# Kernel optimization log

Measured on AMD Instinct MI355X. Metric: run time of the kernel, lower is better.

The kernel has to match this reference:

```python
import jax, jax.numpy as jnp
import numpy as np

N_NODES = 100000
N_EDGES = 640000
D_IN = 128
D_OUT = 128


def setup_inputs() -> dict:
    key = jax.random.key(0)
    k1, k2, k3, k4 = jax.random.split(key, 4)
    x = jax.random.normal(k1, (N_NODES, D_IN), dtype=jnp.float32)
    edge_index = jax.random.randint(k2, (2, N_EDGES), 0, N_NODES, dtype=jnp.int64)
    # nn.Linear(input_dim, out_dim): weight [out, in], bias [out]
    bound = 1.0 / np.sqrt(D_IN)
    W = jax.random.uniform(k3, (D_OUT, D_IN), minval=-bound, maxval=bound, dtype=jnp.float32)
    b = jax.random.uniform(k4, (D_OUT,), minval=-bound, maxval=bound, dtype=jnp.float32)
    return {"x": x, "edge_index": edge_index, "W": W, "b": b}


def reference(x, edge_index, W, b):
    # GINConv (eps=0): h_i = (1+eps)*x_i + sum_{j in N(i)} x_j, then Linear(h)
    src = edge_index[0]
    dst = edge_index[1]
    agg = jax.ops.segment_sum(x[src], dst, num_segments=N_NODES)  # [N, D_IN]
    h = x + agg
    return h @ W.T + b  # [N, D_OUT]
```

## Files before the change

### kernel.cpp

```cpp
#include <hip/hip_runtime.h>
#include <hip/hip_bf16.h>

#define N_NODES 100000
#define N_EDGES 640000
#define D 128
#define NBINS 782
#define NBINSP 784
#define CHB 320
#define CHE 2000
#define CAP 2048
#define GB 1563
#define TB (GB + CHB)

typedef __attribute__((ext_vector_type(8))) short short8;
typedef __attribute__((ext_vector_type(4))) float f32x4;

__device__ __forceinline__ short f32_to_bf16(float f) {
  union { float f; unsigned u; } c; c.f = f;
  unsigned u = c.u;
  unsigned r = (u + 0x7FFFu + ((u >> 16) & 1u)) >> 16;
  return (short)r;
}
__device__ __forceinline__ float lo_bf16(unsigned v) {
  union { unsigned u; float f; } c; c.u = v << 16; return c.f;
}
__device__ __forceinline__ float hi_bf16(unsigned v) {
  union { unsigned u; float f; } c; c.u = v & 0xFFFF0000u; return c.f;
}

__global__ __launch_bounds__(256) void gemm_count(const float* x, const float* W,
                                                  const int* ei, short* y, int* hist) {
  __shared__ char ldsbuf[128 * 136 * 2];
  int b = blockIdx.x;
  int g_incl = ((b + 1) * GB) / TB;
  bool is_gemm = g_incl > (b * GB) / TB;
  int t = threadIdx.x;

  if (!is_gemm) {
    int* h = (int*)ldsbuf;
    int sid = b - g_incl;
    for (int j = t; j < NBINSP; j += 256) h[j] = 0;
    __syncthreads();
    int base = sid * CHE;
    for (int i = t; i < CHE; i += 256) {
      int dst = ei[N_EDGES + base + i];
      atomicAdd(&h[dst >> 7], 1);
    }
    __syncthreads();
    for (int j = t; j < NBINSP; j += 256) hist[sid * NBINSP + j] = h[j];
    return;
  }

  short (*Wlds)[136] = (short(*)[136])ldsbuf;
  int gb = g_incl - 1;
  for (int idx = t * 8; idx < D * D; idx += 256 * 8) {
    int r = idx >> 7, c = idx & 127;
    float4 a = *reinterpret_cast<const float4*>(W + idx);
    float4 bb = *reinterpret_cast<const float4*>(W + idx + 4);
    short8 s;
    s[0] = f32_to_bf16(a.x);  s[1] = f32_to_bf16(a.y);
    s[2] = f32_to_bf16(a.z);  s[3] = f32_to_bf16(a.w);
    s[4] = f32_to_bf16(bb.x); s[5] = f32_to_bf16(bb.y);
    s[6] = f32_to_bf16(bb.z); s[7] = f32_to_bf16(bb.w);
    *reinterpret_cast<short8*>(&Wlds[r][c]) = s;
  }
  __syncthreads();

  int wave = t >> 6, lane = t & 63;
  int l15 = lane & 15, kq = lane >> 4;
  int row0 = gb * 64 + wave * 16;
  if (row0 >= N_NODES) return;
  int ar = row0 + l15;
  if (ar >= N_NODES) ar = N_NODES - 1;
  const float* xrow = x + (size_t)ar * D;

  f32x4 acc[8];
#pragma unroll
  for (int n = 0; n < 8; ++n) acc[n] = (f32x4){0.f, 0.f, 0.f, 0.f};

#pragma unroll
  for (int kk = 0; kk < 4; ++kk) {
    int k0 = kk * 32 + kq * 8;
    float4 a0 = *reinterpret_cast<const float4*>(xrow + k0);
    float4 a1 = *reinterpret_cast<const float4*>(xrow + k0 + 4);
    short8 af;
    af[0] = f32_to_bf16(a0.x); af[1] = f32_to_bf16(a0.y);
    af[2] = f32_to_bf16(a0.z); af[3] = f32_to_bf16(a0.w);
    af[4] = f32_to_bf16(a1.x); af[5] = f32_to_bf16(a1.y);
    af[6] = f32_to_bf16(a1.z); af[7] = f32_to_bf16(a1.w);
#pragma unroll
    for (int n = 0; n < 8; ++n) {
      short8 bf = *reinterpret_cast<short8*>(&Wlds[n * 16 + l15][k0]);
      acc[n] = __builtin_amdgcn_mfma_f32_16x16x32_bf16(af, bf, acc[n], 0, 0, 0);
    }
  }

  int orow0 = row0 + kq * 4;
#pragma unroll
  for (int n = 0; n < 8; ++n) {
#pragma unroll
    for (int r = 0; r < 4; ++r) {
      int row = orow0 + r;
      if (row < N_NODES)
        y[(size_t)row * D + n * 16 + l15] = f32_to_bf16(acc[n][r]);
    }
  }
}

__global__ __launch_bounds__(256) void scan_cols(const int* hist, int* scanned, int* bintot) {
  __shared__ int sdata[256];
  int j = blockIdx.x;
  int t = threadIdx.x;
  int a = 0, b = 0;
  if (t < CHB / 2) {
    a = hist[(2 * t) * NBINSP + j];
    b = hist[(2 * t + 1) * NBINSP + j];
  }
  int ps = a + b;
  sdata[t] = ps;
  __syncthreads();
  int incl = ps;
  for (int off = 1; off < 256; off <<= 1) {
    int u = (t >= off) ? sdata[t - off] : 0;
    __syncthreads();
    incl += u;
    sdata[t] = incl;
    __syncthreads();
  }
  if (t < CHB / 2) {
    int excl = incl - ps;
    scanned[j * CHB + 2 * t] = excl;
    scanned[j * CHB + 2 * t + 1] = excl + a;
  }
  if (t == CHB / 2 - 1) bintot[j] = incl;
}

__global__ __launch_bounds__(256) void scan_bins(const int* bintot, int* bases) {
  __shared__ int sdata[256];
  int t = threadIdx.x;
  int v0 = 0, v1 = 0, v2 = 0, v3 = 0;
  if (t < NBINSP / 4) {
    int4 vv = *reinterpret_cast<const int4*>(bintot + 4 * t);
    v0 = vv.x; v1 = vv.y; v2 = vv.z; v3 = vv.w;
  }
  int s = v0 + v1 + v2 + v3;
  sdata[t] = s;
  __syncthreads();
  int incl = s;
  for (int off = 1; off < 256; off <<= 1) {
    int u = (t >= off) ? sdata[t - off] : 0;
    __syncthreads();
    incl += u;
    sdata[t] = incl;
    __syncthreads();
  }
  if (t < NBINSP / 4) {
    int e = incl - s;
    bases[4 * t + 0] = e;
    bases[4 * t + 1] = e + v0;
    bases[4 * t + 2] = e + v0 + v1;
    bases[4 * t + 3] = e + v0 + v1 + v2;
  }
  if (t == NBINSP / 4 - 1) bases[NBINSP] = incl;
}

__global__ __launch_bounds__(256) void bin_place(const int* ei, const int* scanned,
                                                 const int* bases, int* binned) {
  __shared__ int rk[NBINSP];
  __shared__ int cb[NBINSP];
  int t = threadIdx.x, b = blockIdx.x;
  for (int j = t; j < NBINSP; j += 256) {
    rk[j] = 0;
    cb[j] = bases[j] + scanned[j * CHB + b];
  }
  __syncthreads();
  int base = b * CHE;
  for (int i = t; i < CHE; i += 256) {
    int e = base + i;
    int src = ei[e];
    int dst = ei[N_EDGES + e];
    int bin = dst >> 7;
    int r = atomicAdd(&rk[bin], 1);
    binned[cb[bin] + r] = ((dst & 127) << 17) | src;
  }
}

__global__ __launch_bounds__(256) void sort_bins(const int* binned, const int* bases,
                                                 int* csr, int* nstart, int* ndeg) {
  __shared__ int c[128];
  __shared__ int st[128];
  __shared__ int sdata[128];
  int bin = blockIdx.x, t = threadIdx.x;
  int est = bases[bin];
  int E = bases[bin + 1] - est;
  if (E > CAP) E = CAP;
  if (t < 128) c[t] = 0;
  __syncthreads();

  int pv[8], rv[8];
#pragma unroll
  for (int j = 0; j < 8; ++j) {
    int i = j * 256 + t;
    bool v = i < E;
    int p = v ? binned[est + i] : 0;
    pv[j] = p;
    rv[j] = v ? atomicAdd(&c[p >> 17], 1) : 0;
  }
  __syncthreads();

  if (t < 128) sdata[t] = c[t];
  __syncthreads();
  int incl = (t < 128) ? sdata[t] : 0;
  for (int off = 1; off < 128; off <<= 1) {
    int u = (t >= off && t < 128) ? sdata[t - off] : 0;
    __syncthreads();
    if (t < 128) {
      incl += u;
      sdata[t] = incl;
    }
    __syncthreads();
  }
  if (t < 128) {
    st[t] = incl - c[t];
    int gnode = bin * 128 + t;
    if (gnode < N_NODES) {
      nstart[gnode] = est + st[t];
      ndeg[gnode] = c[t];
    }
  }
  __syncthreads();

#pragma unroll
  for (int j = 0; j < 8; ++j) {
    int i = j * 256 + t;
    if (i < E) {
      int p = pv[j];
      csr[est + st[p >> 17] + rv[j]] = p & 0x1FFFF;
    }
  }
}

__global__ __launch_bounds__(256) void gather_csr(const short* y, const int* nstart,
                                                  const int* ndeg, const int* csr,
                                                  const float* bias, float* out) {
  int gtid = blockIdx.x * 256 + threadIdx.x;
  int wave = gtid >> 6;
  int lane = threadIdx.x & 63;
  int g = lane >> 5;
  int l = lane & 31;
  int node = wave * 2 + g;

  int deg = ndeg[node];
  int start = nstart[node];
  int dcap = deg < 32 ? deg : 32;
  int docap = __shfl_xor(dcap, 32);
  int kmaxw = dcap > docap ? dcap : docap;

  int ids = (l < dcap) ? csr[start + l] : 0;
  int base_sl = lane & 32;

  const uint2* yq = (const uint2*)y;
  uint2 self = yq[(size_t)node * 32 + l];

  float4 acc[8];
#pragma unroll
  for (int i = 0; i < 8; ++i) acc[i] = make_float4(0.f, 0.f, 0.f, 0.f);

  for (int k = 0; k < kmaxw; k += 8) {
#pragma unroll
    for (int i = 0; i < 8; ++i) {
      int kk = k + i;
      int src = __shfl(ids, base_sl + kk);
      uint2 w = yq[(size_t)src * 32 + l];
      bool val = kk < dcap;
      w.x = val ? w.x : 0u;
      w.y = val ? w.y : 0u;
      acc[i].x += lo_bf16(w.x);
      acc[i].y += hi_bf16(w.x);
      acc[i].z += lo_bf16(w.y);
      acc[i].w += hi_bf16(w.y);
    }
  }
  for (int k = 32; k < deg; ++k) {
    int src = csr[start + k];
    uint2 w = yq[(size_t)src * 32 + l];
    acc[0].x += lo_bf16(w.x);
    acc[0].y += hi_bf16(w.x);
    acc[0].z += lo_bf16(w.y);
    acc[0].w += hi_bf16(w.y);
  }

  float4 bv = ((const float4*)bias)[l];
  float4 tot;
  tot.x = (lo_bf16(self.x) + bv.x) + (((acc[0].x + acc[1].x) + (acc[2].x + acc[3].x)) +
                                      ((acc[4].x + acc[5].x) + (acc[6].x + acc[7].x)));
  tot.y = (hi_bf16(self.x) + bv.y) + (((acc[0].y + acc[1].y) + (acc[2].y + acc[3].y)) +
                                      ((acc[4].y + acc[5].y) + (acc[6].y + acc[7].y)));
  tot.z = (lo_bf16(self.y) + bv.z) + (((acc[0].z + acc[1].z) + (acc[2].z + acc[3].z)) +
                                      ((acc[4].z + acc[5].z) + (acc[6].z + acc[7].z)));
  tot.w = (hi_bf16(self.y) + bv.w) + (((acc[0].w + acc[1].w) + (acc[2].w + acc[3].w)) +
                                      ((acc[4].w + acc[5].w) + (acc[6].w + acc[7].w)));

  ((float4*)out)[(size_t)node * 32 + l] = tot;
}

__global__ void copy_x(const float4* x, float4* h, int n4) {
  int i = blockIdx.x * blockDim.x + threadIdx.x;
  int s = gridDim.x * blockDim.x;
  for (; i < n4; i += s) h[i] = x[i];
}

__global__ void scatter_add(const float* x, const int* ei, float* h) {
  int i = blockIdx.x * blockDim.x + threadIdx.x;
  int s = gridDim.x * blockDim.x;
  const int total = N_EDGES * 32;
  for (; i < total; i += s) {
    int e = i >> 5;
    int c = (i & 31) << 2;
    int src = ei[e];
    int dst = ei[N_EDGES + e];
    float4 v = *reinterpret_cast<const float4*>(x + (size_t)src * D + c);
    float* hp = h + (size_t)dst * D + c;
    unsafeAtomicAdd(hp + 0, v.x);
    unsafeAtomicAdd(hp + 1, v.y);
    unsafeAtomicAdd(hp + 2, v.z);
    unsafeAtomicAdd(hp + 3, v.w);
  }
}

__global__ __launch_bounds__(256) void gin_gemm_f32(const float* h, const float* W,
                                                    const float* bias, float* out) {
  __shared__ short Wlds[128][136];
  int t = threadIdx.x;
  for (int idx = t * 8; idx < D * D; idx += 256 * 8) {
    int r = idx >> 7, c = idx & 127;
    float4 a = *reinterpret_cast<const float4*>(W + idx);
    float4 b = *reinterpret_cast<const float4*>(W + idx + 4);
    short8 s;
    s[0] = f32_to_bf16(a.x); s[1] = f32_to_bf16(a.y);
    s[2] = f32_to_bf16(a.z); s[3] = f32_to_bf16(a.w);
    s[4] = f32_to_bf16(b.x); s[5] = f32_to_bf16(b.y);
    s[6] = f32_to_bf16(b.z); s[7] = f32_to_bf16(b.w);
    *reinterpret_cast<short8*>(&Wlds[r][c]) = s;
  }
  __syncthreads();

  int wave = t >> 6, lane = t & 63;
  int l15 = lane & 15, kq = lane >> 4;
  int row0 = blockIdx.x * 64 + wave * 16;
  if (row0 >= N_NODES) return;
  int ar = row0 + l15;
  if (ar >= N_NODES) ar = N_NODES - 1;
  const float* hrow = h + (size_t)ar * D;

  f32x4 acc[8];
#pragma unroll
  for (int n = 0; n < 8; ++n) acc[n] = (f32x4){0.f, 0.f, 0.f, 0.f};

#pragma unroll
  for (int kk = 0; kk < 4; ++kk) {
    int k0 = kk * 32 + kq * 8;
    float4 a0 = *reinterpret_cast<const float4*>(hrow + k0);
    float4 a1 = *reinterpret_cast<const float4*>(hrow + k0 + 4);
    short8 af;
    af[0] = f32_to_bf16(a0.x); af[1] = f32_to_bf16(a0.y);
    af[2] = f32_to_bf16(a0.z); af[3] = f32_to_bf16(a0.w);
    af[4] = f32_to_bf16(a1.x); af[5] = f32_to_bf16(a1.y);
    af[6] = f32_to_bf16(a1.z); af[7] = f32_to_bf16(a1.w);
#pragma unroll
    for (int n = 0; n < 8; ++n) {
      short8 bf = *reinterpret_cast<short8*>(&Wlds[n * 16 + l15][k0]);
      acc[n] = __builtin_amdgcn_mfma_f32_16x16x32_bf16(af, bf, acc[n], 0, 0, 0);
    }
  }

  int orow0 = row0 + kq * 4;
#pragma unroll
  for (int n = 0; n < 8; ++n) {
    float bv = bias[n * 16 + l15];
#pragma unroll
    for (int r = 0; r < 4; ++r) {
      int row = orow0 + r;
      if (row < N_NODES)
        out[(size_t)row * D + n * 16 + l15] = acc[n][r] + bv;
    }
  }
}

extern "C" void kernel_launch(void* const* d_in, const int* in_sizes, int n_in,
                              void* d_out, int out_size, void* d_ws, size_t ws_size,
                              hipStream_t stream) {
  const float* x   = (const float*)d_in[0];
  const int*   ei  = (const int*)d_in[1];
  const float* W   = (const float*)d_in[2];
  const float* bia = (const float*)d_in[3];
  float* out = (float*)d_out;
  (void)in_sizes; (void)n_in; (void)out_size;

  const size_t HIST_I   = (size_t)CHB * NBINSP;
  const size_t SCAN_I   = (size_t)NBINSP * CHB;
  const size_t BINTOT_I = NBINSP;
  const size_t BASES_I  = 800;
  const size_t BINNED_I = N_EDGES;
  const size_t CSR_I    = N_EDGES;
  const size_t NST_I    = N_NODES;
  const size_t NDG_I    = N_NODES;
  const size_t INTS = HIST_I + SCAN_I + BINTOT_I + BASES_I + BINNED_I + CSR_I + NST_I + NDG_I;
  const size_t Y_B  = (size_t)N_NODES * D * 2;
  const size_t NEED = INTS * 4 + Y_B;

  if (ws_size >= NEED) {
    int* hist    = (int*)d_ws;
    int* scanned = hist + HIST_I;
    int* bintot  = scanned + SCAN_I;
    int* bases   = bintot + BINTOT_I;
    int* binned  = bases + BASES_I;
    int* csr     = binned + BINNED_I;
    int* nstart  = csr + CSR_I;
    int* ndeg    = nstart + NST_I;
    short* y     = (short*)(ndeg + NDG_I);

    gemm_count<<<TB, 256, 0, stream>>>(x, W, ei, y, hist);
    scan_cols<<<NBINSP, 256, 0, stream>>>(hist, scanned, bintot);
    scan_bins<<<1, 256, 0, stream>>>(bintot, bases);
    bin_place<<<CHB, 256, 0, stream>>>(ei, scanned, bases, binned);
    sort_bins<<<NBINS, 256, 0, stream>>>(binned, bases, csr, nstart, ndeg);
    gather_csr<<<(N_NODES / 2) / 4, 256, 0, stream>>>(y, nstart, ndeg, csr, bia, out);
  } else {
    int n4 = N_NODES * D / 4;
    copy_x<<<(n4 + 255) / 256, 256, 0, stream>>>((const float4*)x, (float4*)out, n4);
    int total = N_EDGES * 32;
    scatter_add<<<(total + 255) / 256, 256, 0, stream>>>(x, ei, out);
    gin_gemm_f32<<<(N_NODES + 63) / 64, 256, 0, stream>>>(out, W, bia, out);
  }
}
```

Measured before the change: 89.66 us.

## Distribute GEMM tiles across all CSR-build phase kernels to fill idle CUs

```diff
diff --git a/kernel.cpp b/kernel.cpp
--- a/kernel.cpp
+++ b/kernel.cpp
@@ -9,8 +9,12 @@
 #define CHB 320
 #define CHE 2000
 #define CAP 2048
-#define GB 1563
-#define TB (GB + CHB)
+#define GBT 1563
+#define G1 300
+#define G2 300
+#define G3 200
+#define G4 350
+#define G5 413
 
 typedef __attribute__((ext_vector_type(8))) short short8;
 typedef __attribute__((ext_vector_type(4))) float f32x4;
@@ -28,31 +32,10 @@
   union { unsigned u; float f; } c; c.u = v & 0xFFFF0000u; return c.f;
 }
 
-__global__ __launch_bounds__(256) void gemm_count(const float* x, const float* W,
-                                                  const int* ei, short* y, int* hist) {
-  __shared__ char ldsbuf[128 * 136 * 2];
-  int b = blockIdx.x;
-  int g_incl = ((b + 1) * GB) / TB;
-  bool is_gemm = g_incl > (b * GB) / TB;
-  int t = threadIdx.x;
-
-  if (!is_gemm) {
-    int* h = (int*)ldsbuf;
-    int sid = b - g_incl;
-    for (int j = t; j < NBINSP; j += 256) h[j] = 0;
-    __syncthreads();
-    int base = sid * CHE;
-    for (int i = t; i < CHE; i += 256) {
-      int dst = ei[N_EDGES + base + i];
-      atomicAdd(&h[dst >> 7], 1);
-    }
-    __syncthreads();
-    for (int j = t; j < NBINSP; j += 256) hist[sid * NBINSP + j] = h[j];
-    return;
-  }
-
+__device__ __forceinline__ void gemm_body(const float* x, const float* W, short* y,
+                                          int gb, char* ldsbuf) {
   short (*Wlds)[136] = (short(*)[136])ldsbuf;
-  int gb = g_incl - 1;
+  int t = threadIdx.x;
   for (int idx = t * 8; idx < D * D; idx += 256 * 8) {
     int r = idx >> 7, c = idx & 127;
     float4 a = *reinterpret_cast<const float4*>(W + idx);
@@ -107,16 +90,47 @@
   }
 }
 
-__global__ __launch_bounds__(256) void scan_cols(const int* hist, int* scanned, int* bintot) {
-  __shared__ int sdata[256];
-  int j = blockIdx.x;
-  int t = threadIdx.x;
-  int a = 0, b = 0;
+#define HETERO_MAP(S_, G_)                                   \
+  int b = blockIdx.x;                                        \
+  int g_incl = ((b + 1) * (G_)) / ((S_) + (G_));             \
+  bool is_gemm = g_incl > (b * (G_)) / ((S_) + (G_));        \
+  int sid = b - g_incl;                                      \
+  int gb_loc = g_incl - 1;
+
+__global__ __launch_bounds__(256) void p1_count(const float* x, const float* W, short* y,
+                                                const int* ei, int* hist) {
+  __shared__ char ldsbuf[34816];
+  HETERO_MAP(CHB, G1)
+  int t = threadIdx.x;
+  if (is_gemm) { gemm_body(x, W, y, gb_loc, ldsbuf); return; }
+
+  int* h = (int*)ldsbuf;
+  for (int j = t; j < NBINSP; j += 256) h[j] = 0;
+  __syncthreads();
+  int base = sid * CHE;
+  for (int i = t; i < CHE; i += 256) {
+    int dst = ei[N_EDGES + base + i];
+    atomicAdd(&h[dst >> 7], 1);
+  }
+  __syncthreads();
+  for (int j = t; j < NBINSP; j += 256) hist[sid * NBINSP + j] = h[j];
+}
+
+__global__ __launch_bounds__(256) void p2_scancols(const float* x, const float* W, short* y,
+                                                   const int* hist, int* scanned, int* bintot) {
+  __shared__ char ldsbuf[34816];
+  HETERO_MAP(NBINSP, G2)
+  int t = threadIdx.x;
+  if (is_gemm) { gemm_body(x, W, y, G1 + gb_loc, ldsbuf); return; }
+
+  int* sdata = (int*)ldsbuf;
+  int j = sid;
+  int a = 0, bb = 0;
   if (t < CHB / 2) {
     a = hist[(2 * t) * NBINSP + j];
-    b = hist[(2 * t + 1) * NBINSP + j];
-  }
-  int ps = a + b;
+    bb = hist[(2 * t + 1) * NBINSP + j];
+  }
+  int ps = a + bb;
   sdata[t] = ps;
   __syncthreads();
   int incl = ps;
@@ -135,9 +149,14 @@
   if (t == CHB / 2 - 1) bintot[j] = incl;
 }
 
-__global__ __launch_bounds__(256) void scan_bins(const int* bintot, int* bases) {
-  __shared__ int sdata[256];
-  int t = threadIdx.x;
+__global__ __launch_bounds__(256) void p3_scanbins(const float* x, const float* W, short* y,
+                                                   const int* bintot, int* bases) {
+  __shared__ char ldsbuf[34816];
+  int b = blockIdx.x;
+  int t = threadIdx.x;
+  if (b > 0) { gemm_body(x, W, y, G1 + G2 + b - 1, ldsbuf); return; }
+
+  int* sdata = (int*)ldsbuf;
   int v0 = 0, v1 = 0, v2 = 0, v3 = 0;
   if (t < NBINSP / 4) {
     int4 vv = *reinterpret_cast<const int4*>(bintot + 4 * t);
@@ -164,17 +183,22 @@
   if (t == NBINSP / 4 - 1) bases[NBINSP] = incl;
 }
 
-__global__ __launch_bounds__(256) void bin_place(const int* ei, const int* scanned,
-                                                 const int* bases, int* binned) {
-  __shared__ int rk[NBINSP];
-  __shared__ int cb[NBINSP];
-  int t = threadIdx.x, b = blockIdx.x;
+__global__ __launch_bounds__(256) void p4_place(const float* x, const float* W, short* y,
+                                                const int* ei, const int* scanned,
+                                                const int* bases, int* binned) {
+  __shared__ char ldsbuf[34816];
+  HETERO_MAP(CHB, G4)
+  int t = threadIdx.x;
+  if (is_gemm) { gemm_body(x, W, y, G1 + G2 + G3 + gb_loc, ldsbuf); return; }
+
+  int* rk = (int*)ldsbuf;
+  int* cb = rk + NBINSP;
   for (int j = t; j < NBINSP; j += 256) {
     rk[j] = 0;
-    cb[j] = bases[j] + scanned[j * CHB + b];
-  }
-  __syncthreads();
-  int base = b * CHE;
+    cb[j] = bases[j] + scanned[j * CHB + sid];
+  }
+  __syncthreads();
+  int base = sid * CHE;
   for (int i = t; i < CHE; i += 256) {
     int e = base + i;
     int src = ei[e];
@@ -185,12 +209,18 @@
   }
 }
 
-__global__ __launch_bounds__(256) void sort_bins(const int* binned, const int* bases,
-                                                 int* csr, int* nstart, int* ndeg) {
-  __shared__ int c[128];
-  __shared__ int st[128];
-  __shared__ int sdata[128];
-  int bin = blockIdx.x, t = threadIdx.x;
+__global__ __launch_bounds__(256) void p5_sort(const float* x, const float* W, short* y,
+                                               const int* binned, const int* bases,
+                                               int* csr, int* nstart, int* ndeg) {
+  __shared__ char ldsbuf[34816];
+  HETERO_MAP(NBINS, G5)
+  int t = threadIdx.x;
+  if (is_gemm) { gemm_body(x, W, y, G1 + G2 + G3 + G4 + gb_loc, ldsbuf); return; }
+
+  int* c = (int*)ldsbuf;
+  int* st = c + 128;
+  int* sdata = st + 128;
+  int bin = sid;
   int est = bases[bin];
   int E = bases[bin + 1] - est;
   if (E > CAP) E = CAP;
@@ -420,12 +450,12 @@
     int* ndeg    = nstart + NST_I;
     short* y     = (short*)(ndeg + NDG_I);
 
-    gemm_count<<<TB, 256, 0, stream>>>(x, W, ei, y, hist);
-    scan_cols<<<NBINSP, 256, 0, stream>>>(hist, scanned, bintot);
-    scan_bins<<<1, 256, 0, stream>>>(bintot, bases);
-    bin_place<<<CHB, 256, 0, stream>>>(ei, scanned, bases, binned);
-    sort_bins<<<NBINS, 256, 0, stream>>>(binned, bases, csr, nstart, ndeg);
-    gather_csr<<<(N_NODES / 2) / 4, 256, 0, stream>>>(y, nstart, ndeg, csr, bia, out);
+    p1_count   <<<CHB + G1,    256, 0, stream>>>(x, W, y, ei, hist);
+    p2_scancols<<<NBINSP + G2, 256, 0, stream>>>(x, W, y, hist, scanned, bintot);
+    p3_scanbins<<<1 + G3,      256, 0, stream>>>(x, W, y, bintot, bases);
+    p4_place   <<<CHB + G4,    256, 0, stream>>>(x, W, y, ei, scanned, bases, binned);
+    p5_sort    <<<NBINS + G5,  256, 0, stream>>>(x, W, y, binned, bases, csr, nstart, ndeg);
+    gather_csr <<<(N_NODES / 2) / 4, 256, 0, stream>>>(y, nstart, ndeg, csr, bia, out);
   } else {
     int n4 = N_NODES * D / 4;
     copy_x<<<(n4 + 255) / 256, 256, 0, stream>>>((const float4*)x, (float4*)out, n4);
```

Measured after the change: 96.24 us. +7.3%, slower.

## Replace CSR with fixed 32-slot padded adjacency and zero-row sentinel

Applied to the files above, without the earlier changes.

```diff
diff --git a/kernel.cpp b/kernel.cpp
--- a/kernel.cpp
+++ b/kernel.cpp
@@ -11,6 +11,8 @@
 #define CAP 2048
 #define GB 1563
 #define TB (GB + CHB)
+#define ZROW N_NODES
+#define CSRN (NBINS * 128)
 
 typedef __attribute__((ext_vector_type(8))) short short8;
 typedef __attribute__((ext_vector_type(4))) float f32x4;
@@ -135,9 +137,11 @@
   if (t == CHB / 2 - 1) bintot[j] = incl;
 }
 
-__global__ __launch_bounds__(256) void scan_bins(const int* bintot, int* bases) {
+__global__ __launch_bounds__(256) void scan_bins(const int* bintot, int* bases, short* y) {
   __shared__ int sdata[256];
   int t = threadIdx.x;
+  if (t < 64) ((int*)(y + (size_t)ZROW * D))[t] = 0;
+
   int v0 = 0, v1 = 0, v2 = 0, v3 = 0;
   if (t < NBINSP / 4) {
     int4 vv = *reinterpret_cast<const int4*>(bintot + 4 * t);
@@ -185,64 +189,43 @@
   }
 }
 
-__global__ __launch_bounds__(256) void sort_bins(const int* binned, const int* bases,
-                                                 int* csr, int* nstart, int* ndeg) {
+__global__ __launch_bounds__(256) void sort_bins32(const int* binned, const int* bases,
+                                                   int* csr32, int* ndeg) {
   __shared__ int c[128];
-  __shared__ int st[128];
-  __shared__ int sdata[128];
   int bin = blockIdx.x, t = threadIdx.x;
+  if (t < 128) c[t] = 0;
+  __syncthreads();
   int est = bases[bin];
   int E = bases[bin + 1] - est;
   if (E > CAP) E = CAP;
-  if (t < 128) c[t] = 0;
-  __syncthreads();
-
-  int pv[8], rv[8];
-#pragma unroll
-  for (int j = 0; j < 8; ++j) {
-    int i = j * 256 + t;
-    bool v = i < E;
-    int p = v ? binned[est + i] : 0;
-    pv[j] = p;
-    rv[j] = v ? atomicAdd(&c[p >> 17], 1) : 0;
-  }
-  __syncthreads();
-
-  if (t < 128) sdata[t] = c[t];
-  __syncthreads();
-  int incl = (t < 128) ? sdata[t] : 0;
-  for (int off = 1; off < 128; off <<= 1) {
-    int u = (t >= off && t < 128) ? sdata[t - off] : 0;
-    __syncthreads();
-    if (t < 128) {
-      incl += u;
-      sdata[t] = incl;
-    }
-    __syncthreads();
-  }
-  if (t < 128) {
-    st[t] = incl - c[t];
-    int gnode = bin * 128 + t;
-    if (gnode < N_NODES) {
-      nstart[gnode] = est + st[t];
-      ndeg[gnode] = c[t];
-    }
-  }
-  __syncthreads();
 
 #pragma unroll
   for (int j = 0; j < 8; ++j) {
     int i = j * 256 + t;
     if (i < E) {
-      int p = pv[j];
-      csr[est + st[p >> 17] + rv[j]] = p & 0x1FFFF;
-    }
-  }
-}
-
-__global__ __launch_bounds__(256) void gather_csr(const short* y, const int* nstart,
-                                                  const int* ndeg, const int* csr,
-                                                  const float* bias, float* out) {
+      int p = binned[est + i];
+      int off = p >> 17;
+      int r = atomicAdd(&c[off], 1);
+      if (r < 32)
+        csr32[(size_t)((bin << 7) + off) * 32 + r] = p & 0x1FFFF;
+    }
+  }
+  __syncthreads();
+
+  if (t < 128) {
+    int gnode = (bin << 7) + t;
+    if (gnode < N_NODES) ndeg[gnode] = c[t];
+  }
+  for (int s = t; s < 128 * 32; s += 256) {
+    int node = s >> 5, slot = s & 31;
+    if (slot >= c[node])
+      csr32[(size_t)((bin << 7) + node) * 32 + slot] = ZROW;
+  }
+}
+
+__global__ __launch_bounds__(256) void gather32(const short* y, const int* ndeg,
+                                                const int* csr32, const float* bias,
+                                                float* out) {
   int gtid = blockIdx.x * 256 + threadIdx.x;
   int wave = gtid >> 6;
   int lane = threadIdx.x & 63;
@@ -251,12 +234,11 @@
   int node = wave * 2 + g;
 
   int deg = ndeg[node];
-  int start = nstart[node];
-  int dcap = deg < 32 ? deg : 32;
-  int docap = __shfl_xor(dcap, 32);
-  int kmaxw = dcap > docap ? dcap : docap;
-
-  int ids = (l < dcap) ? csr[start + l] : 0;
+  if (deg > 32) deg = 32;
+  int dother = __shfl_xor(deg, 32);
+  int kmaxw = deg > dother ? deg : dother;
+
+  int ids = csr32[(size_t)node * 32 + l];
   int base_sl = lane & 32;
 
   const uint2* yq = (const uint2*)y;
@@ -269,25 +251,13 @@
   for (int k = 0; k < kmaxw; k += 8) {
 #pragma unroll
     for (int i = 0; i < 8; ++i) {
-      int kk = k + i;
-      int src = __shfl(ids, base_sl + kk);
+      int src = __shfl(ids, base_sl + k + i);
       uint2 w = yq[(size_t)src * 32 + l];
-      bool val = kk < dcap;
-      w.x = val ? w.x : 0u;
-      w.y = val ? w.y : 0u;
       acc[i].x += lo_bf16(w.x);
       acc[i].y += hi_bf16(w.x);
       acc[i].z += lo_bf16(w.y);
       acc[i].w += hi_bf16(w.y);
     }
-  }
-  for (int k = 32; k < deg; ++k) {
-    int src = csr[start + k];
-    uint2 w = yq[(size_t)src * 32 + l];
-    acc[0].x += lo_bf16(w.x);
-    acc[0].y += hi_bf16(w.x);
-    acc[0].z += lo_bf16(w.y);
-    acc[0].w += hi_bf16(w.y);
   }
 
   float4 bv = ((const float4*)bias)[l];
@@ -402,11 +372,10 @@
   const size_t BINTOT_I = NBINSP;
   const size_t BASES_I  = 800;
   const size_t BINNED_I = N_EDGES;
-  const size_t CSR_I    = N_EDGES;
-  const size_t NST_I    = N_NODES;
-  const size_t NDG_I    = N_NODES;
-  const size_t INTS = HIST_I + SCAN_I + BINTOT_I + BASES_I + BINNED_I + CSR_I + NST_I + NDG_I;
-  const size_t Y_B  = (size_t)N_NODES * D * 2;
+  const size_t CSR_I    = (size_t)CSRN * 32;
+  const size_t NDG_I    = CSRN;
+  const size_t INTS = HIST_I + SCAN_I + BINTOT_I + BASES_I + BINNED_I + CSR_I + NDG_I;
+  const size_t Y_B  = (size_t)(N_NODES + 1) * D * 2;
   const size_t NEED = INTS * 4 + Y_B;
 
   if (ws_size >= NEED) {
@@ -415,17 +384,16 @@
     int* bintot  = scanned + SCAN_I;
     int* bases   = bintot + BINTOT_I;
     int* binned  = bases + BASES_I;
-    int* csr     = binned + BINNED_I;
-    int* nstart  = csr + CSR_I;
-    int* ndeg    = nstart + NST_I;
+    int* csr32   = binned + BINNED_I;
+    int* ndeg    = csr32 + CSR_I;
     short* y     = (short*)(ndeg + NDG_I);
 
-    gemm_count<<<TB, 256, 0, stream>>>(x, W, ei, y, hist);
-    scan_cols<<<NBINSP, 256, 0, stream>>>(hist, scanned, bintot);
-    scan_bins<<<1, 256, 0, stream>>>(bintot, bases);
-    bin_place<<<CHB, 256, 0, stream>>>(ei, scanned, bases, binned);
-    sort_bins<<<NBINS, 256, 0, stream>>>(binned, bases, csr, nstart, ndeg);
-    gather_csr<<<(N_NODES / 2) / 4, 256, 0, stream>>>(y, nstart, ndeg, csr, bia, out);
+    gemm_count <<<TB, 256, 0, stream>>>(x, W, ei, y, hist);
+    scan_cols  <<<NBINSP, 256, 0, stream>>>(hist, scanned, bintot);
+    scan_bins  <<<1, 256, 0, stream>>>(bintot, bases, y);
+    bin_place  <<<CHB, 256, 0, stream>>>(ei, scanned, bases, binned);
+    sort_bins32<<<NBINS, 256, 0, stream>>>(binned, bases, csr32, ndeg);
+    gather32   <<<(N_NODES / 2) / 4, 256, 0, stream>>>(y, ndeg, csr32, bia, out);
   } else {
     int n4 = N_NODES * D / 4;
     copy_x<<<(n4 + 255) / 256, 256, 0, stream>>>((const float4*)x, (float4*)out, n4);
```

Result: slower. 92.17 us (+2.8%).
